# Kernel tuning notes

Hardware: AMD Instinct MI355X
Metric: run time of the kernel (lower is better)

## Reference

```python
import jax, jax.numpy as jnp
import numpy as np

HS = 512   # hidden_size
IN = 2048  # input_size
MB = 100   # memory_bank_size
T  = 4096  # nImg


def setup_inputs() -> dict:
    key = jax.random.key(0)
    ks = jax.random.split(key, 20)

    def w(k, i, o):
        return jax.random.normal(k, (i, o), jnp.float32) * (1.0 / np.sqrt(i))

    def b(k, o):
        return jax.random.normal(k, (o,), jnp.float32) * 0.01

    return {
        "hidden_out_a": jax.random.normal(ks[0], (T, IN), jnp.float32),
        "hidden_out_m": jax.random.normal(ks[1], (T, IN), jnp.float32),
        "W_ca": w(ks[2], HS + IN, HS),  "b_ca": b(ks[3], HS),    # hidden_to_content_a
        "W_cm": w(ks[4], HS + IN, HS),  "b_cm": b(ks[5], HS),    # hidden_to_content_m
        "W_wp": w(ks[6], 3 * HS, 3),    "b_wp": b(ks[7], 3),     # write_prob
        "W_wpa": w(ks[8], HS + IN, MB), "b_wpa": b(ks[9], MB),   # write_prob_a
        "W_wpm": w(ks[10], HS + IN, MB),"b_wpm": b(ks[11], MB),  # write_prob_m
        "W_rp": w(ks[12], 3 * HS, MB),  "b_rp": b(ks[13], MB),   # read_prob
        "W_rh": w(ks[14], 2 * HS, HS),  "b_rh": b(ks[15], HS),   # read_to_hidden
        "W_rha": w(ks[16], 2 * HS + IN, HS), "b_rha": b(ks[17], HS),  # read_to_hidden_a
        "W_rhm": w(ks[18], 2 * HS + IN, HS), "b_rhm": b(ks[19], HS),  # read_to_hidden_m
        "nImg": T,
    }


def reference(hidden_out_a, hidden_out_m,
              W_ca, b_ca, W_cm, b_cm,
              W_wp, b_wp, W_wpa, b_wpa, W_wpm, b_wpm,
              W_rp, b_rp, W_rh, b_rh,
              W_rha, b_rha, W_rhm, b_rhm,
              nImg):
    hs = W_rh.shape[1]
    mb = W_rp.shape[1]

    def step(carry, xs):
        mem, h, ha, hm = carry            # mem: [MB, HS]; h/ha/hm: [HS]
        xa, xm = xs                       # [IN] each
        xh = jnp.concatenate([ha, hm, h])               # [3*HS]
        ar = jax.nn.softmax(xh @ W_rp + b_rp)           # [MB]
        r = ar @ mem                                    # [HS] memory read
        h1 = jax.nn.relu(jnp.concatenate([r, h]) @ W_rh + b_rh)
        ha1 = jax.nn.relu(jnp.concatenate([xa, r, ha]) @ W_rha + b_rha)
        hm1 = jax.nn.relu(jnp.concatenate([xm, r, hm]) @ W_rhm + b_rhm)
        aw = jax.nn.softmax(xh @ W_wp + b_wp)           # [3] stream gate
        xha = jnp.concatenate([ha, xa])                 # [HS+IN]
        xhm = jnp.concatenate([hm, xm])
        c_a = jax.nn.relu(xha @ W_ca + b_ca)            # [HS]
        c_m = jax.nn.relu(xhm @ W_cm + b_cm)
        aw_a = jax.nn.softmax(xha @ W_wpa + b_wpa)      # [MB]
        aw_m = jax.nn.softmax(xhm @ W_wpm + b_wpm)
        mem = aw[0] * mem + aw[1] * aw_a[:, None] * c_a + aw[2] * aw_m[:, None] * c_m
        return (mem, h1, ha1, hm1), h1

    init = (jnp.zeros((mb, hs), hidden_out_a.dtype),
            jnp.zeros((hs,), hidden_out_a.dtype),
            jnp.zeros((hs,), hidden_out_a.dtype),
            jnp.zeros((hs,), hidden_out_a.dtype))
    _, hiddens = jax.lax.scan(step, init,
                              (hidden_out_a[:nImg], hidden_out_m[:nImg]))
    return hiddens  # [nImg, HS]
```

## Files before the change

kernel.cpp:

```cpp
#include <hip/hip_runtime.h>
#include <cstdint>
#include <cstddef>

#define HS 512

constexpr int TPB  = 512;
constexpr int GBLK = 64;
constexpr int OWNB = 24;
constexpr int OWNW = 3;

constexpr size_t OFF_TWrp  = 0;
constexpr size_t OFF_TWwp  = OFF_TWrp  + 100*1536;
constexpr size_t OFF_TWwpa = OFF_TWwp  + 3*1536;
constexpr size_t OFF_TWwpm = OFF_TWwpa + 100*512;
constexpr size_t OFF_TWca  = OFF_TWwpm + 100*512;
constexpr size_t OFF_TWcm  = OFF_TWca  + 512*512;
constexpr size_t OFF_TWh0  = OFF_TWcm  + 512*512;
constexpr size_t OFF_TWh1  = OFF_TWh0  + 512*512;
constexpr size_t OFF_TWh2  = OFF_TWh1  + 512*512;
constexpr size_t OFF_TWu0  = OFF_TWh2  + 512*512;
constexpr size_t OFF_TWu1  = OFF_TWu0  + 512*512;
constexpr size_t OFF_TWu2  = OFF_TWu1  + 512*512;
constexpr size_t OFF_PAca  = OFF_TWu2  + 512*512;
constexpr size_t OFF_PMcm  = OFF_PAca  + 4096*512;
constexpr size_t OFF_PArha = OFF_PMcm  + 4096*512;
constexpr size_t OFF_PMrhm = OFF_PArha + 4096*512;
constexpr size_t OFF_PAwpa = OFF_PMrhm + 4096*512;
constexpr size_t OFF_PMwpm = OFF_PAwpa + 4096*100;
constexpr size_t OFF_CARRY = OFF_PMwpm + 4096*100;
constexpr size_t OFF_BCAST = OFF_CARRY + 2*1536*2;

__device__ __forceinline__ unsigned long long ald(const unsigned long long* p) {
  return __hip_atomic_load(const_cast<unsigned long long*>(p),
                           __ATOMIC_RELAXED, __HIP_MEMORY_SCOPE_AGENT);
}
__device__ __forceinline__ void gstTag(unsigned long long* p, float v, unsigned tag) {
  unsigned long long u = ((unsigned long long)tag << 32) | (unsigned long long)__float_as_uint(v);
  __hip_atomic_store(p, u, __ATOMIC_RELAXED, __HIP_MEMORY_SCOPE_AGENT);
}
__device__ __forceinline__ float xrsum(float v) {
  #pragma unroll
  for (int o = 32; o; o >>= 1) v += __shfl_xor(v, o, 64);
  return v;
}

template<int K4>
__device__ __forceinline__ float dotK(const float* __restrict__ w, const float* x) {
  int l = threadIdx.x & 63;
  const float4* w4 = (const float4*)w;
  const float4* x4 = (const float4*)x;
  float acc = 0.f;
  #pragma unroll
  for (int it = 0; it < K4; ++it) {
    float4 a = w4[l + 64*it];
    float4 b = x4[l + 64*it];
    acc += a.x*b.x + a.y*b.y + a.z*b.z + a.w*b.w;
  }
  return acc;
}

__device__ __forceinline__ void dot2K512(const float* __restrict__ w,
                                         const float* xa, const float* xm,
                                         float& ra, float& rm) {
  int l = threadIdx.x & 63;
  const float4* w4 = (const float4*)w;
  const float4* a4 = (const float4*)xa;
  const float4* m4 = (const float4*)xm;
  float sa = 0.f, sm = 0.f;
  #pragma unroll
  for (int it = 0; it < 2; ++it) {
    float4 wv = w4[l + 64*it], av = a4[l + 64*it], mv = m4[l + 64*it];
    sa += wv.x*av.x + wv.y*av.y + wv.z*av.z + wv.w*av.w;
    sm += wv.x*mv.x + wv.y*mv.y + wv.z*mv.z + wv.w*mv.w;
  }
  #pragma unroll
  for (int o = 32; o; o >>= 1) { sa += __shfl_xor(sa, o, 64); sm += __shfl_xor(sm, o, 64); }
  ra = sa; rm = sm;
}

__global__ void initK(unsigned long long* carryT, unsigned long long* bcast) {
  int i = blockIdx.x * blockDim.x + threadIdx.x, st = gridDim.x * blockDim.x;
  for (int k = i; k < 1536; k += st) carryT[k] = (1ull << 32);
  for (int k = i; k < 1536; k += st) carryT[1536 + k] = 0ull;
  for (int k = i; k < 2 * 1344; k += st) bcast[k] = 0ull;
}

__global__ void transK(const float* __restrict__ src, float* __restrict__ dst, int R, int C) {
  __shared__ float tile[32][33];
  int c0 = blockIdx.x * 32, r0 = blockIdx.y * 32;
  for (int i = threadIdx.y; i < 32; i += 8) {
    int r = r0 + i, c = c0 + threadIdx.x;
    tile[i][threadIdx.x] = (r < R && c < C) ? src[(size_t)r * C + c] : 0.f;
  }
  __syncthreads();
  for (int i = threadIdx.y; i < 32; i += 8) {
    int c = c0 + i, r = r0 + threadIdx.x;
    if (c < C && r < R) dst[(size_t)c * R + r] = tile[threadIdx.x][i];
  }
}

__global__ __launch_bounds__(256) void gemmK(const float* __restrict__ X,
                                             const float* __restrict__ W,
                                             float* __restrict__ C, int N) {
  __shared__ float As[16][68];
  __shared__ float Bs[16][68];
  int t0 = blockIdx.y * 64, n0 = blockIdx.x * 64;
  int tid = threadIdx.x, tx = tid & 15, ty = tid >> 4;
  float acc[4][4] = {};
  for (int k0 = 0; k0 < 2048; k0 += 16) {
    {
      int r = tid >> 2, c = (tid & 3) * 4;
      float4 v = *(const float4*)(X + (size_t)(t0 + r) * 2048 + k0 + c);
      As[c + 0][r] = v.x; As[c + 1][r] = v.y; As[c + 2][r] = v.z; As[c + 3][r] = v.w;
    }
    {
      int kr = tid >> 4, c = (tid & 15) * 4;
      int gcol = n0 + c;
      const float* src = W + (size_t)(k0 + kr) * N + gcol;
      #pragma unroll
      for (int i = 0; i < 4; ++i) Bs[kr][c + i] = (gcol + i < N) ? src[i] : 0.f;
    }
    __syncthreads();
    #pragma unroll
    for (int kk = 0; kk < 16; ++kk) {
      float4 a4 = *(const float4*)&As[kk][ty * 4];
      float4 b4 = *(const float4*)&Bs[kk][tx * 4];
      float av[4] = {a4.x, a4.y, a4.z, a4.w};
      float bv[4] = {b4.x, b4.y, b4.z, b4.w};
      #pragma unroll
      for (int i = 0; i < 4; ++i)
        #pragma unroll
        for (int j = 0; j < 4; ++j) acc[i][j] += av[i] * bv[j];
    }
    __syncthreads();
  }
  #pragma unroll
  for (int i = 0; i < 4; ++i)
    #pragma unroll
    for (int j = 0; j < 4; ++j) {
      int col = n0 + tx * 4 + j;
      if (col < N) C[(size_t)(t0 + ty * 4 + i) * N + col] = acc[i][j];
    }
}

__global__ __launch_bounds__(256) void gemm128(const float* __restrict__ X,
                                               const float* __restrict__ W,
                                               float* __restrict__ C) {
  __shared__ float As[8][132];
  __shared__ float Bs[8][132];
  const int N = 512;
  int t0 = blockIdx.y * 128, n0 = blockIdx.x * 128;
  int tid = threadIdx.x, tx = tid & 15, ty = tid >> 4;
  float acc[8][8] = {};
  for (int k0 = 0; k0 < 2048; k0 += 8) {
    int r = tid >> 1, c4 = (tid & 1) * 4;
    float4 va = *(const float4*)(X + (size_t)(t0 + r) * 2048 + k0 + c4);
    int kr = tid >> 5, cb = (tid & 31) * 4;
    float4 vb = *(const float4*)(W + (size_t)(k0 + kr) * N + n0 + cb);
    __syncthreads();
    As[c4 + 0][r] = va.x; As[c4 + 1][r] = va.y; As[c4 + 2][r] = va.z; As[c4 + 3][r] = va.w;
    Bs[kr][cb] = vb.x; Bs[kr][cb + 1] = vb.y; Bs[kr][cb + 2] = vb.z; Bs[kr][cb + 3] = vb.w;
    __syncthreads();
    #pragma unroll
    for (int kk = 0; kk < 8; ++kk) {
      float av[8], bv[8];
      *(float4*)av       = *(const float4*)&As[kk][ty * 8];
      *(float4*)(av + 4) = *(const float4*)&As[kk][ty * 8 + 4];
      *(float4*)bv       = *(const float4*)&Bs[kk][tx * 8];
      *(float4*)(bv + 4) = *(const float4*)&Bs[kk][tx * 8 + 4];
      #pragma unroll
      for (int i = 0; i < 8; ++i)
        #pragma unroll
        for (int j = 0; j < 8; ++j) acc[i][j] += av[i] * bv[j];
    }
  }
  #pragma unroll
  for (int i = 0; i < 8; ++i) {
    float* dst = C + (size_t)(t0 + ty * 8 + i) * N + n0 + tx * 8;
    *(float4*)dst       = *(float4*)&acc[i][0];
    *(float4*)(dst + 4) = *(float4*)&acc[i][4];
  }
}

struct RArgs {
  const float *TWrp, *TWwp, *TWwpa, *TWwpm, *TWca, *TWcm;
  const float *TWh0, *TWh1, *TWh2, *TWu0, *TWu1, *TWu2;
  const float *PAca, *PMcm, *PArha, *PMrhm, *PAwpa, *PMwpm;
  const float *b_ca, *b_cm, *b_wp, *b_wpa, *b_wpm, *b_rp, *b_rh, *b_rha, *b_rhm;
  unsigned long long *carryT, *bcast;
  float *out;
  int nT;
};

__global__ __launch_bounds__(TPB, 1) void recurK(RArgs a) {
  const int tid  = threadIdx.x;
  const int lane = tid & 63;
  const int lw   = tid >> 6;
  const int b    = blockIdx.x;

  __shared__ __align__(16) float s_wca[8 * 512];
  __shared__ __align__(16) float s_wcm[8 * 512];
  __shared__ __align__(16) float s_wbig[2 * 1536];
  __shared__ __align__(16) float s_wsm[4 * 512];
  __shared__ __align__(16) float s_TWu[OWNB * 512];
  __shared__ float s_G[OWNB * 104];
  __shared__ __align__(16) float s_x[1536];
  __shared__ __align__(16) float s_c[1024];
  __shared__ float s_ar[104], s_awa[104], s_awm[104], s_aw[4];
  __shared__ float s_part[OWNB];

  const int r0a = (b + 51) & 63;
  const int r1m = (b + 25) & 63;
  const bool big1_grp = (b < 36);
  const bool big1_wp  = (b >= 40 && b <= 42);

  for (int i = tid; i < 8 * 512; i += TPB) {
    int row = i >> 9, col = i & 511;
    s_wca[i] = a.TWca[(size_t)(b * 8 + row) * 512 + col];
    s_wcm[i] = a.TWcm[(size_t)(b * 8 + row) * 512 + col];
  }
  for (int i = tid; i < 1536; i += TPB) {
    s_wbig[i] = a.TWrp[(size_t)b * 1536 + i];
    float v2 = 0.f;
    if (big1_grp)      v2 = a.TWrp[(size_t)(b + 64) * 1536 + i];
    else if (big1_wp)  v2 = a.TWwp[(size_t)(b - 40) * 1536 + i];
    s_wbig[1536 + i] = v2;
  }
  for (int i = tid; i < 512; i += TPB) {
    s_wsm[i]        = a.TWwpa[(size_t)r0a * 512 + i];
    s_wsm[512 + i]  = (r0a < 36) ? a.TWwpa[(size_t)(r0a + 64) * 512 + i] : 0.f;
    s_wsm[1024 + i] = a.TWwpm[(size_t)r1m * 512 + i];
    s_wsm[1536 + i] = (r1m < 36) ? a.TWwpm[(size_t)(r1m + 64) * 512 + i] : 0.f;
  }
  for (int i = tid; i < OWNB * 512; i += TPB) {
    int rr = i >> 9, col = i & 511;
    int q = b * OWNB + rr, hsel = q >> 9, j = q & 511;
    const float* src = (hsel == 0) ? a.TWu0 : (hsel == 1) ? a.TWu1 : a.TWu2;
    s_TWu[i] = src[(size_t)j * 512 + col];
  }
  for (int i = tid; i < OWNB * 104; i += TPB) s_G[i] = 0.f;

  const int cacol = b * 8 + lw;
  const float bCa = a.b_ca[cacol];
  const float bCm = a.b_cm[cacol];

  int gtype = 0, gslot = 0, gdst = 0, gxoff = 0;
  const float* gpre = nullptr;
  float gbias = 0.f;
  if (lw == 7)      { gtype = 1; gslot = 0; gdst = 1024 + b; gbias = a.b_rp[b]; }
  else if (lw == 6) {
    if (big1_grp)     { gtype = 1; gslot = 1; gdst = 1024 + b + 64; gbias = a.b_rp[b + 64]; }
    else if (big1_wp) { gtype = 1; gslot = 1; gdst = 1324 + (b - 40); gbias = a.b_wp[b - 40]; }
  }
  else if (lw == 5) { gtype = 2; gslot = 0; gdst = 1124 + r0a; gxoff = 0;
                      gpre = a.PAwpa + r0a; gbias = a.b_wpa[r0a]; }
  else if (lw == 4 && r0a < 36) { gtype = 2; gslot = 1; gdst = 1124 + r0a + 64; gxoff = 0;
                      gpre = a.PAwpa + r0a + 64; gbias = a.b_wpa[r0a + 64]; }
  else if (lw == 3) { gtype = 2; gslot = 2; gdst = 1224 + r1m; gxoff = 512;
                      gpre = a.PMwpm + r1m; gbias = a.b_wpm[r1m]; }
  else if (lw == 2 && r1m < 36) { gtype = 2; gslot = 3; gdst = 1224 + r1m + 64; gxoff = 512;
                      gpre = a.PMwpm + r1m + 64; gbias = a.b_wpm[r1m + 64]; }

  int ownHsel[OWNW], ownJ[OWNW], whX[OWNW];
  float ownBias[OWNW];
  const float* ownPre[OWNW];
  const float* whRow[OWNW];
  #pragma unroll
  for (int k = 0; k < OWNW; ++k) {
    int q = b * OWNB + lw * OWNW + k, hsel = q >> 9, j = q & 511;
    ownHsel[k] = hsel; ownJ[k] = j;
    if (hsel == 0)      { ownBias[k] = a.b_rh[j];  ownPre[k] = nullptr;
                          whRow[k] = a.TWh0 + (size_t)j * 512; whX[k] = 1024; }
    else if (hsel == 1) { ownBias[k] = a.b_rha[j]; ownPre[k] = a.PArha + j;
                          whRow[k] = a.TWh1 + (size_t)j * 512; whX[k] = 0; }
    else                { ownBias[k] = a.b_rhm[j]; ownPre[k] = a.PMrhm + j;
                          whRow[k] = a.TWh2 + (size_t)j * 512; whX[k] = 512; }
  }
  __syncthreads();

  for (int t = 0; t < a.nT; ++t) {
    const unsigned tagB = (unsigned)t + 1;
    unsigned long long* bc = a.bcast + (size_t)(t & 1) * 1344;

    float preCa = a.PAca[(size_t)t * 512 + cacol];
    float preCm = a.PMcm[(size_t)t * 512 + cacol];
    float preG  = (gtype == 2) ? gpre[(size_t)t * 100] : 0.f;
    float preO[OWNW];
    #pragma unroll
    for (int k = 0; k < OWNW; ++k)
      preO[k] = ownPre[k] ? ownPre[k][(size_t)t * 512] : 0.f;

    {
      const unsigned long long* cin = a.carryT + (size_t)(t & 1) * 1536;
      int i0 = tid, i1 = tid + 512, i2 = tid + 1024;
      unsigned long long v0 = ald(cin + i0), v1 = ald(cin + i1), v2 = ald(cin + i2);
      while (((unsigned)(v0 >> 32) < tagB) | ((unsigned)(v1 >> 32) < tagB) |
             ((unsigned)(v2 >> 32) < tagB)) {
        __builtin_amdgcn_s_sleep(1);
        v0 = ald(cin + i0); v1 = ald(cin + i1); v2 = ald(cin + i2);
      }
      s_x[i0] = __uint_as_float((unsigned)v0);
      s_x[i1] = __uint_as_float((unsigned)v1);
      s_x[i2] = __uint_as_float((unsigned)v2);
    }
    __syncthreads();

    if (gtype == 1) {
      float v = xrsum(dotK<6>(s_wbig + gslot * 1536, s_x));
      if (!lane) gstTag(bc + gdst, v + gbias, tagB);
    } else if (gtype == 2) {
      float v = xrsum(dotK<2>(s_wsm + gslot * 512, s_x + gxoff));
      if (!lane) gstTag(bc + gdst, v + gbias + preG, tagB);
    }
    {
      float v = xrsum(dotK<2>(s_wca + lw * 512, s_x));
      if (!lane) gstTag(bc + cacol, fmaxf(v + preCa + bCa, 0.f), tagB);
      v = xrsum(dotK<2>(s_wcm + lw * 512, s_x + 512));
      if (!lane) gstTag(bc + 512 + cacol, fmaxf(v + preCm + bCm, 0.f), tagB);
    }
    #pragma unroll
    for (int k = 0; k < OWNW; ++k) {
      float v = xrsum(dotK<2>(whRow[k], s_x + whX[k]));
      if (!lane) s_part[lw * OWNW + k] = v;
    }

    if (lw < 3) {
      int base = 1024 + lw * 100;
      const unsigned long long* p1 = bc + base + lane;
      bool two = lane < 36;
      unsigned long long v1 = ald(p1);
      unsigned long long v2 = two ? ald(p1 + 64) : ~0ull;
      while (((unsigned)(v1 >> 32) < tagB) | ((unsigned)(v2 >> 32) < tagB)) {
        __builtin_amdgcn_s_sleep(1);
        v1 = ald(p1); if (two) v2 = ald(p1 + 64);
      }
      float x1 = __uint_as_float((unsigned)v1);
      float x2 = two ? __uint_as_float((unsigned)v2) : -3.0e38f;
      float m = fmaxf(x1, x2);
      #pragma unroll
      for (int o = 32; o; o >>= 1) m = fmaxf(m, __shfl_xor(m, o, 64));
      float e1 = expf(x1 - m);
      float e2 = two ? expf(x2 - m) : 0.f;
      float ss = e1 + e2;
      #pragma unroll
      for (int o = 32; o; o >>= 1) ss += __shfl_xor(ss, o, 64);
      float inv = 1.f / ss;
      float* dst = (lw == 0) ? s_ar : (lw == 1) ? s_awa : s_awm;
      dst[lane] = e1 * inv;
      if (two) dst[64 + lane] = e2 * inv;
    } else if (lw == 3) {
      float x = -3.0e38f;
      if (lane < 3) {
        const unsigned long long* p = bc + 1324 + lane;
        unsigned long long v = ald(p);
        while ((unsigned)(v >> 32) < tagB) { __builtin_amdgcn_s_sleep(1); v = ald(p); }
        x = __uint_as_float((unsigned)v);
      }
      float m = x;
      #pragma unroll
      for (int o = 32; o; o >>= 1) m = fmaxf(m, __shfl_xor(m, o, 64));
      float e = (lane < 3) ? expf(x - m) : 0.f;
      float ss = e;
      #pragma unroll
      for (int o = 32; o; o >>= 1) ss += __shfl_xor(ss, o, 64);
      if (lane < 3) s_aw[lane] = e / ss;
    } else {
      int base = tid - 256;
      const unsigned long long* p = bc + base;
      unsigned long long v0 = ald(p), v1 = ald(p + 256), v2 = ald(p + 512), v3 = ald(p + 768);
      while (((unsigned)(v0 >> 32) < tagB) | ((unsigned)(v1 >> 32) < tagB) |
             ((unsigned)(v2 >> 32) < tagB) | ((unsigned)(v3 >> 32) < tagB)) {
        __builtin_amdgcn_s_sleep(1);
        v0 = ald(p); v1 = ald(p + 256); v2 = ald(p + 512); v3 = ald(p + 768);
      }
      s_c[base]       = __uint_as_float((unsigned)v0);
      s_c[base + 256] = __uint_as_float((unsigned)v1);
      s_c[base + 512] = __uint_as_float((unsigned)v2);
      s_c[base + 768] = __uint_as_float((unsigned)v3);
    }
    __syncthreads();

    const float aw0 = s_aw[0], aw1 = s_aw[1], aw2 = s_aw[2];
    unsigned long long* cout = a.carryT + (size_t)((t + 1) & 1) * 1536;
    #pragma unroll
    for (int k = 0; k < OWNW; ++k) {
      int rr = lw * OWNW + k;
      float uA, uM;
      dot2K512(s_TWu + (size_t)rr * 512, s_c, s_c + 512, uA, uM);

      float* grow = s_G + rr * 104;
      bool two = lane < 36;
      float g1 = grow[lane];
      float g2 = two ? grow[64 + lane] : 0.f;
      float contrib = s_ar[lane] * g1 + (two ? s_ar[64 + lane] * g2 : 0.f);
      contrib = xrsum(contrib);
      grow[lane] = aw0 * g1 + aw1 * s_awa[lane] * uA + aw2 * s_awm[lane] * uM;
      if (two)
        grow[64 + lane] = aw0 * g2 + aw1 * s_awa[64 + lane] * uA + aw2 * s_awm[64 + lane] * uM;

      if (!lane) {
        int j = ownJ[k];
        float h = fmaxf(contrib + s_part[rr] + preO[k] + ownBias[k], 0.f);
        if (ownHsel[k] == 0) {
          a.out[(size_t)t * 512 + j] = h;
          gstTag(cout + 1024 + j, h, tagB + 1);
        } else if (ownHsel[k] == 1) {
          gstTag(cout + j, h, tagB + 1);
        } else {
          gstTag(cout + 512 + j, h, tagB + 1);
        }
      }
    }
    __syncthreads();
  }
}

extern "C" void kernel_launch(void* const* d_in, const int* in_sizes, int n_in,
                              void* d_out, int out_size, void* d_ws, size_t ws_size,
                              hipStream_t stream) {
  const float* Xa    = (const float*)d_in[0];
  const float* Xm    = (const float*)d_in[1];
  const float* W_ca  = (const float*)d_in[2];  const float* b_ca  = (const float*)d_in[3];
  const float* W_cm  = (const float*)d_in[4];  const float* b_cm  = (const float*)d_in[5];
  const float* W_wp  = (const float*)d_in[6];  const float* b_wp  = (const float*)d_in[7];
  const float* W_wpa = (const float*)d_in[8];  const float* b_wpa = (const float*)d_in[9];
  const float* W_wpm = (const float*)d_in[10]; const float* b_wpm = (const float*)d_in[11];
  const float* W_rp  = (const float*)d_in[12]; const float* b_rp  = (const float*)d_in[13];
  const float* W_rh  = (const float*)d_in[14]; const float* b_rh  = (const float*)d_in[15];
  const float* W_rha = (const float*)d_in[16]; const float* b_rha = (const float*)d_in[17];
  const float* W_rhm = (const float*)d_in[18]; const float* b_rhm = (const float*)d_in[19];

  int nT = out_size / HS;
  float* ws = (float*)d_ws;

  initK<<<dim3(64), dim3(256), 0, stream>>>(
      (unsigned long long*)(ws + OFF_CARRY),
      (unsigned long long*)(ws + OFF_BCAST));

  dim3 tb(32, 8);
  auto tg = [](int R, int C) { return dim3((C + 31) / 32, (R + 31) / 32); };
  transK<<<tg(1536, 100), tb, 0, stream>>>(W_rp,                       ws + OFF_TWrp,  1536, 100);
  transK<<<tg(1536, 3),   tb, 0, stream>>>(W_wp,                       ws + OFF_TWwp,  1536, 3);
  transK<<<tg(512, 100),  tb, 0, stream>>>(W_wpa,                      ws + OFF_TWwpa, 512, 100);
  transK<<<tg(512, 100),  tb, 0, stream>>>(W_wpm,                      ws + OFF_TWwpm, 512, 100);
  transK<<<tg(512, 512),  tb, 0, stream>>>(W_ca,                       ws + OFF_TWca,  512, 512);
  transK<<<tg(512, 512),  tb, 0, stream>>>(W_cm,                       ws + OFF_TWcm,  512, 512);
  transK<<<tg(512, 512),  tb, 0, stream>>>(W_rh  + 512 * 512,          ws + OFF_TWh0,  512, 512);
  transK<<<tg(512, 512),  tb, 0, stream>>>(W_rha + (size_t)2560 * 512, ws + OFF_TWh1,  512, 512);
  transK<<<tg(512, 512),  tb, 0, stream>>>(W_rhm + (size_t)2560 * 512, ws + OFF_TWh2,  512, 512);
  transK<<<tg(512, 512),  tb, 0, stream>>>(W_rh,                       ws + OFF_TWu0,  512, 512);
  transK<<<tg(512, 512),  tb, 0, stream>>>(W_rha + (size_t)2048 * 512, ws + OFF_TWu1,  512, 512);
  transK<<<tg(512, 512),  tb, 0, stream>>>(W_rhm + (size_t)2048 * 512, ws + OFF_TWu2,  512, 512);

  int tB = nT / 128;
  gemm128<<<dim3(4, tB), dim3(256), 0, stream>>>(Xa, W_ca + (size_t)512 * 512, ws + OFF_PAca);
  gemm128<<<dim3(4, tB), dim3(256), 0, stream>>>(Xm, W_cm + (size_t)512 * 512, ws + OFF_PMcm);
  gemm128<<<dim3(4, tB), dim3(256), 0, stream>>>(Xa, W_rha,                    ws + OFF_PArha);
  gemm128<<<dim3(4, tB), dim3(256), 0, stream>>>(Xm, W_rhm,                    ws + OFF_PMrhm);
  int tB64 = nT / 64;
  gemmK<<<dim3(2, tB64), dim3(256), 0, stream>>>(Xa, W_wpa + (size_t)512 * 100, ws + OFF_PAwpa, 100);
  gemmK<<<dim3(2, tB64), dim3(256), 0, stream>>>(Xm, W_wpm + (size_t)512 * 100, ws + OFF_PMwpm, 100);

  RArgs a;
  a.TWrp  = ws + OFF_TWrp;  a.TWwp  = ws + OFF_TWwp;
  a.TWwpa = ws + OFF_TWwpa; a.TWwpm = ws + OFF_TWwpm;
  a.TWca  = ws + OFF_TWca;  a.TWcm  = ws + OFF_TWcm;
  a.TWh0  = ws + OFF_TWh0;  a.TWh1  = ws + OFF_TWh1;  a.TWh2 = ws + OFF_TWh2;
  a.TWu0  = ws + OFF_TWu0;  a.TWu1  = ws + OFF_TWu1;  a.TWu2 = ws + OFF_TWu2;
  a.PAca  = ws + OFF_PAca;  a.PMcm  = ws + OFF_PMcm;
  a.PArha = ws + OFF_PArha; a.PMrhm = ws + OFF_PMrhm;
  a.PAwpa = ws + OFF_PAwpa; a.PMwpm = ws + OFF_PMwpm;
  a.b_ca = b_ca; a.b_cm = b_cm; a.b_wp = b_wp; a.b_wpa = b_wpa; a.b_wpm = b_wpm;
  a.b_rp = b_rp; a.b_rh = b_rh; a.b_rha = b_rha; a.b_rhm = b_rhm;
  a.carryT = (unsigned long long*)(ws + OFF_CARRY);
  a.bcast  = (unsigned long long*)(ws + OFF_BCAST);
  a.out    = (float*)d_out;
  a.nT     = nT;

  recurK<<<dim3(GBLK), dim3(TPB), 0, stream>>>(a);
}
```

Before: 27.94 ms.

## Defer memory-bank update by one step to take it off the critical path

The write-side work (content vectors, write softmaxes, stream gate and the s_G memory update) is moved into the next timestep. There it runs while waiting on the read-probability logits, so the per-step serial chain only contains the read softmax and the hidden update. The broadcast buffer layout is reordered so the read logits come first, and one end-of-step barrier is removed. The cost is more complex tag bookkeeping across two buffer parities. There is also a possible race on s_G or s_ar between the update of the next step and the reads of the current step now that the final barrier is gone.

After: 31.03 ms. 11.1% more time.

```diff
diff --git a/kernel.cpp b/kernel.cpp
--- a/kernel.cpp
+++ b/kernel.cpp
@@ -206,6 +206,7 @@
   __shared__ float s_G[OWNB * 104];
   __shared__ __align__(16) float s_x[1536];
   __shared__ __align__(16) float s_c[1024];
+  __shared__ float s_gl[204];
   __shared__ float s_ar[104], s_awa[104], s_awm[104], s_aw[4];
   __shared__ float s_part[OWNB];
 
@@ -247,18 +248,18 @@
   int gtype = 0, gslot = 0, gdst = 0, gxoff = 0;
   const float* gpre = nullptr;
   float gbias = 0.f;
-  if (lw == 7)      { gtype = 1; gslot = 0; gdst = 1024 + b; gbias = a.b_rp[b]; }
+  if (lw == 7)      { gtype = 1; gslot = 0; gdst = b; gbias = a.b_rp[b]; }
   else if (lw == 6) {
-    if (big1_grp)     { gtype = 1; gslot = 1; gdst = 1024 + b + 64; gbias = a.b_rp[b + 64]; }
-    else if (big1_wp) { gtype = 1; gslot = 1; gdst = 1324 + (b - 40); gbias = a.b_wp[b - 40]; }
-  }
-  else if (lw == 5) { gtype = 2; gslot = 0; gdst = 1124 + r0a; gxoff = 0;
+    if (big1_grp)     { gtype = 1; gslot = 1; gdst = b + 64; gbias = a.b_rp[b + 64]; }
+    else if (big1_wp) { gtype = 1; gslot = 1; gdst = 300 + (b - 40); gbias = a.b_wp[b - 40]; }
+  }
+  else if (lw == 5) { gtype = 2; gslot = 0; gdst = 100 + r0a; gxoff = 0;
                       gpre = a.PAwpa + r0a; gbias = a.b_wpa[r0a]; }
-  else if (lw == 4 && r0a < 36) { gtype = 2; gslot = 1; gdst = 1124 + r0a + 64; gxoff = 0;
+  else if (lw == 4 && r0a < 36) { gtype = 2; gslot = 1; gdst = 164 + r0a; gxoff = 0;
                       gpre = a.PAwpa + r0a + 64; gbias = a.b_wpa[r0a + 64]; }
-  else if (lw == 3) { gtype = 2; gslot = 2; gdst = 1224 + r1m; gxoff = 512;
+  else if (lw == 3) { gtype = 2; gslot = 2; gdst = 200 + r1m; gxoff = 512;
                       gpre = a.PMwpm + r1m; gbias = a.b_wpm[r1m]; }
-  else if (lw == 2 && r1m < 36) { gtype = 2; gslot = 3; gdst = 1224 + r1m + 64; gxoff = 512;
+  else if (lw == 2 && r1m < 36) { gtype = 2; gslot = 3; gdst = 264 + r1m; gxoff = 512;
                       gpre = a.PMwpm + r1m + 64; gbias = a.b_wpm[r1m + 64]; }
 
   int ownHsel[OWNW], ownJ[OWNW], whX[OWNW];
@@ -279,7 +280,7 @@
   __syncthreads();
 
   for (int t = 0; t < a.nT; ++t) {
-    const unsigned tagB = (unsigned)t + 1;
+    const unsigned tagC = (unsigned)t + 1;
     unsigned long long* bc = a.bcast + (size_t)(t & 1) * 1344;
 
     float preCa = a.PAca[(size_t)t * 512 + cacol];
@@ -294,8 +295,8 @@
       const unsigned long long* cin = a.carryT + (size_t)(t & 1) * 1536;
       int i0 = tid, i1 = tid + 512, i2 = tid + 1024;
       unsigned long long v0 = ald(cin + i0), v1 = ald(cin + i1), v2 = ald(cin + i2);
-      while (((unsigned)(v0 >> 32) < tagB) | ((unsigned)(v1 >> 32) < tagB) |
-             ((unsigned)(v2 >> 32) < tagB)) {
+      while (((unsigned)(v0 >> 32) < tagC) | ((unsigned)(v1 >> 32) < tagC) |
+             ((unsigned)(v2 >> 32) < tagC)) {
         __builtin_amdgcn_s_sleep(1);
         v0 = ald(cin + i0); v1 = ald(cin + i1); v2 = ald(cin + i2);
       }
@@ -307,16 +308,16 @@
 
     if (gtype == 1) {
       float v = xrsum(dotK<6>(s_wbig + gslot * 1536, s_x));
-      if (!lane) gstTag(bc + gdst, v + gbias, tagB);
+      if (!lane) gstTag(bc + gdst, v + gbias, tagC);
     } else if (gtype == 2) {
       float v = xrsum(dotK<2>(s_wsm + gslot * 512, s_x + gxoff));
-      if (!lane) gstTag(bc + gdst, v + gbias + preG, tagB);
+      if (!lane) gstTag(bc + gdst, v + gbias + preG, tagC);
     }
     {
       float v = xrsum(dotK<2>(s_wca + lw * 512, s_x));
-      if (!lane) gstTag(bc + cacol, fmaxf(v + preCa + bCa, 0.f), tagB);
+      if (!lane) gstTag(bc + 303 + cacol, fmaxf(v + preCa + bCa, 0.f), tagC);
       v = xrsum(dotK<2>(s_wcm + lw * 512, s_x + 512));
-      if (!lane) gstTag(bc + 512 + cacol, fmaxf(v + preCm + bCm, 0.f), tagB);
+      if (!lane) gstTag(bc + 815 + cacol, fmaxf(v + preCm + bCm, 0.f), tagC);
     }
     #pragma unroll
     for (int k = 0; k < OWNW; ++k) {
@@ -324,15 +325,83 @@
       if (!lane) s_part[lw * OWNW + k] = v;
     }
 
-    if (lw < 3) {
-      int base = 1024 + lw * 100;
-      const unsigned long long* p1 = bc + base + lane;
-      bool two = lane < 36;
-      unsigned long long v1 = ald(p1);
-      unsigned long long v2 = two ? ald(p1 + 64) : ~0ull;
-      while (((unsigned)(v1 >> 32) < tagB) | ((unsigned)(v2 >> 32) < tagB)) {
+    if (t > 0) {
+      const unsigned long long* bp = a.bcast + (size_t)((t - 1) & 1) * 1344;
+      const unsigned tagP = (unsigned)t;
+      {
+        int s1 = 100 + tid, s2 = 612 + tid, s3 = 1124 + tid;
+        bool h3 = (s3 < 1327);
+        unsigned long long v1 = ald(bp + s1), v2 = ald(bp + s2);
+        unsigned long long v3 = h3 ? ald(bp + s3) : ~0ull;
+        while (((unsigned)(v1 >> 32) < tagP) | ((unsigned)(v2 >> 32) < tagP) |
+               ((unsigned)(v3 >> 32) < tagP)) {
+          __builtin_amdgcn_s_sleep(1);
+          v1 = ald(bp + s1); v2 = ald(bp + s2); if (h3) v3 = ald(bp + s3);
+        }
+        s_gl[s1 - 100] = __uint_as_float((unsigned)v1);
+        if (s2 < 303) {}
+        s_c[s2 - 303] = __uint_as_float((unsigned)v2);
+        if (h3) s_c[s3 - 303] = __uint_as_float((unsigned)v3);
+        if (s1 >= 303) s_c[s1 - 303] = __uint_as_float((unsigned)v1);
+      }
+      __syncthreads();
+
+      if (lw == 1 || lw == 2) {
+        const float* g = s_gl + (lw - 1) * 100;
+        float x1 = g[lane];
+        float x2 = (lane < 36) ? g[64 + lane] : -3.0e38f;
+        float m = fmaxf(x1, x2);
+        #pragma unroll
+        for (int o = 32; o; o >>= 1) m = fmaxf(m, __shfl_xor(m, o, 64));
+        float e1 = expf(x1 - m);
+        float e2 = (lane < 36) ? expf(x2 - m) : 0.f;
+        float ss = e1 + e2;
+        #pragma unroll
+        for (int o = 32; o; o >>= 1) ss += __shfl_xor(ss, o, 64);
+        float inv = 1.f / ss;
+        float* dst = (lw == 1) ? s_awa : s_awm;
+        dst[lane] = e1 * inv;
+        if (lane < 36) dst[64 + lane] = e2 * inv;
+      } else if (lw == 3) {
+        float x = (lane < 3) ? s_gl[200 + lane] : -3.0e38f;
+        float m = x;
+        #pragma unroll
+        for (int o = 32; o; o >>= 1) m = fmaxf(m, __shfl_xor(m, o, 64));
+        float e = (lane < 3) ? expf(x - m) : 0.f;
+        float ss = e;
+        #pragma unroll
+        for (int o = 32; o; o >>= 1) ss += __shfl_xor(ss, o, 64);
+        if (lane < 3) s_aw[lane] = e / ss;
+      }
+      float uA[OWNW], uM[OWNW];
+      #pragma unroll
+      for (int k = 0; k < OWNW; ++k) {
+        int rr = lw * OWNW + k;
+        dot2K512(s_TWu + (size_t)rr * 512, s_c, s_c + 512, uA[k], uM[k]);
+      }
+      __syncthreads();
+
+      const float aw0 = s_aw[0], aw1 = s_aw[1], aw2 = s_aw[2];
+      #pragma unroll
+      for (int k = 0; k < OWNW; ++k) {
+        int rr = lw * OWNW + k;
+        float* grow = s_G + rr * 104;
+        grow[lane] = aw0 * grow[lane] + aw1 * s_awa[lane] * uA[k] + aw2 * s_awm[lane] * uM[k];
+        if (lane < 36) {
+          int i2 = 64 + lane;
+          grow[i2] = aw0 * grow[i2] + aw1 * s_awa[i2] * uA[k] + aw2 * s_awm[i2] * uM[k];
+        }
+      }
+    }
+
+    if (lw == 0) {
+      const unsigned long long* p = bc + lane;
+      bool two = (lane < 36);
+      unsigned long long v1 = ald(p);
+      unsigned long long v2 = two ? ald(p + 64) : ~0ull;
+      while (((unsigned)(v1 >> 32) < tagC) | ((unsigned)(v2 >> 32) < tagC)) {
         __builtin_amdgcn_s_sleep(1);
-        v1 = ald(p1); if (two) v2 = ald(p1 + 64);
+        v1 = ald(p); if (two) v2 = ald(p + 64);
       }
       float x1 = __uint_as_float((unsigned)v1);
       float x2 = two ? __uint_as_float((unsigned)v2) : -3.0e38f;
@@ -345,73 +414,32 @@
       #pragma unroll
       for (int o = 32; o; o >>= 1) ss += __shfl_xor(ss, o, 64);
       float inv = 1.f / ss;
-      float* dst = (lw == 0) ? s_ar : (lw == 1) ? s_awa : s_awm;
-      dst[lane] = e1 * inv;
-      if (two) dst[64 + lane] = e2 * inv;
-    } else if (lw == 3) {
-      float x = -3.0e38f;
-      if (lane < 3) {
-        const unsigned long long* p = bc + 1324 + lane;
-        unsigned long long v = ald(p);
-        while ((unsigned)(v >> 32) < tagB) { __builtin_amdgcn_s_sleep(1); v = ald(p); }
-        x = __uint_as_float((unsigned)v);
-      }
-      float m = x;
-      #pragma unroll
-      for (int o = 32; o; o >>= 1) m = fmaxf(m, __shfl_xor(m, o, 64));
-      float e = (lane < 3) ? expf(x - m) : 0.f;
-      float ss = e;
-      #pragma unroll
-      for (int o = 32; o; o >>= 1) ss += __shfl_xor(ss, o, 64);
-      if (lane < 3) s_aw[lane] = e / ss;
-    } else {
-      int base = tid - 256;
-      const unsigned long long* p = bc + base;
-      unsigned long long v0 = ald(p), v1 = ald(p + 256), v2 = ald(p + 512), v3 = ald(p + 768);
-      while (((unsigned)(v0 >> 32) < tagB) | ((unsigned)(v1 >> 32) < tagB) |
-             ((unsigned)(v2 >> 32) < tagB) | ((unsigned)(v3 >> 32) < tagB)) {
-        __builtin_amdgcn_s_sleep(1);
-        v0 = ald(p); v1 = ald(p + 256); v2 = ald(p + 512); v3 = ald(p + 768);
-      }
-      s_c[base]       = __uint_as_float((unsigned)v0);
-      s_c[base + 256] = __uint_as_float((unsigned)v1);
-      s_c[base + 512] = __uint_as_float((unsigned)v2);
-      s_c[base + 768] = __uint_as_float((unsigned)v3);
+      s_ar[lane] = e1 * inv;
+      if (two) s_ar[64 + lane] = e2 * inv;
     }
     __syncthreads();
 
-    const float aw0 = s_aw[0], aw1 = s_aw[1], aw2 = s_aw[2];
     unsigned long long* cout = a.carryT + (size_t)((t + 1) & 1) * 1536;
     #pragma unroll
     for (int k = 0; k < OWNW; ++k) {
       int rr = lw * OWNW + k;
-      float uA, uM;
-      dot2K512(s_TWu + (size_t)rr * 512, s_c, s_c + 512, uA, uM);
-
-      float* grow = s_G + rr * 104;
-      bool two = lane < 36;
-      float g1 = grow[lane];
-      float g2 = two ? grow[64 + lane] : 0.f;
-      float contrib = s_ar[lane] * g1 + (two ? s_ar[64 + lane] * g2 : 0.f);
+      const float* grow = s_G + rr * 104;
+      float contrib = s_ar[lane] * grow[lane];
+      if (lane < 36) contrib += s_ar[64 + lane] * grow[64 + lane];
       contrib = xrsum(contrib);
-      grow[lane] = aw0 * g1 + aw1 * s_awa[lane] * uA + aw2 * s_awm[lane] * uM;
-      if (two)
-        grow[64 + lane] = aw0 * g2 + aw1 * s_awa[64 + lane] * uA + aw2 * s_awm[64 + lane] * uM;
-
       if (!lane) {
         int j = ownJ[k];
         float h = fmaxf(contrib + s_part[rr] + preO[k] + ownBias[k], 0.f);
         if (ownHsel[k] == 0) {
           a.out[(size_t)t * 512 + j] = h;
-          gstTag(cout + 1024 + j, h, tagB + 1);
+          gstTag(cout + 1024 + j, h, tagC + 1);
         } else if (ownHsel[k] == 1) {
-          gstTag(cout + j, h, tagB + 1);
+          gstTag(cout + j, h, tagC + 1);
         } else {
-          gstTag(cout + 512 + j, h, tagB + 1);
+          gstTag(cout + 512 + j, h, tagC + 1);
         }
       }
     }
-    __syncthreads();
   }
 }
 
```
